# Performance work log

Hardware: AMD Instinct MI355X
Metric: run time of the kernel (lower is better)

## Reference

```python
import jax, jax.numpy as jnp
import numpy as np

N_NODES = 100000
N_EDGES = 1600000
D_IN = 128
D_HID = 128


def setup_inputs() -> dict:
    key = jax.random.key(0)
    ks = jax.random.split(key, 7)
    s_in = 1.0 / np.sqrt(D_IN)
    s_hid = 1.0 / np.sqrt(D_HID)
    return {
        "x": jax.random.normal(ks[0], (N_NODES, D_IN), dtype=jnp.float32),
        "edge_index": jax.random.randint(ks[1], (2, N_EDGES), 0, N_NODES, dtype=jnp.int64),
        "W1_l": jax.random.normal(ks[2], (D_IN, D_HID), dtype=jnp.float32) * s_in,
        "b1": jnp.zeros((D_HID,), dtype=jnp.float32),
        "W1_r": jax.random.normal(ks[3], (D_IN, D_HID), dtype=jnp.float32) * s_in,
        "W2_l": jax.random.normal(ks[4], (D_HID, D_HID), dtype=jnp.float32) * s_hid,
        "b2": jnp.zeros((D_HID,), dtype=jnp.float32),
        "W2_r": jax.random.normal(ks[5], (D_HID, D_HID), dtype=jnp.float32) * s_hid,
    }


def _mean_aggregate(x, src, dst, num_nodes):
    # messages x[src] mean-aggregated at dst (PyG SAGEConv default aggr='mean')
    msg = jnp.take(x, src, axis=0)                       # [E, D] gather
    summed = jax.ops.segment_sum(msg, dst, num_segments=num_nodes)  # [N, D]
    deg = jax.ops.segment_sum(jnp.ones((src.shape[0],), x.dtype), dst,
                              num_segments=num_nodes)
    return summed / jnp.maximum(deg, 1.0)[:, None]


def _sage_conv(x, src, dst, W_l, b, W_r):
    agg = _mean_aggregate(x, src, dst, x.shape[0])
    # out = lin_l(aggregated neighbors) + lin_r(root)
    return agg @ W_l + b + x @ W_r


def reference(x, edge_index, W1_l, b1, W1_r, W2_l, b2, W2_r):
    src, dst = edge_index[0], edge_index[1]
    h = _sage_conv(x, src, dst, W1_l, b1, W1_r)
    h = jax.nn.relu(h)  # dropout inactive in eval mode
    out = _sage_conv(h, src, dst, W2_l, b2, W2_r)
    return out
```

## Files before the change

### kernel.cpp

```cpp
#include <hip/hip_runtime.h>

#define NN 100000
#define NE 1600000
#define DF 128
#define NBUCK 391
#define PA_BLOCKS 196
#define PB_BLOCKS 196
#define CX_BLOCKS 3125
#define CW_BLOCKS 64
#define AGG_GRID 3128

typedef short short8 __attribute__((ext_vector_type(8)));
typedef float floatx4 __attribute__((ext_vector_type(4)));
typedef float floatx2 __attribute__((ext_vector_type(2)));
typedef unsigned int uintx4 __attribute__((ext_vector_type(4)));
typedef unsigned int uintx2 __attribute__((ext_vector_type(2)));
typedef unsigned int uint;
typedef unsigned short ushort;
typedef unsigned char uchar;

static __device__ __forceinline__ ushort f2bf(float f) {
    uint u = __builtin_bit_cast(uint, f);
    return (ushort)((u + 0x7fffu + ((u >> 16) & 1u)) >> 16);
}

__global__ __launch_bounds__(256) void pA_hist(const int* __restrict__ dst,
                                               int* __restrict__ hist,
                                               ushort* __restrict__ rank8) {
    __shared__ int h[NBUCK];
    int tid = threadIdx.x;
    for (int i = tid; i < NBUCK; i += 256) h[i] = 0;
    __syncthreads();
    int eb = blockIdx.x * 8192 + tid;
    #pragma unroll
    for (int k = 0; k < 32; ++k) {
        int e = eb + k * 256;
        if (e < NE) {
            int r = atomicAdd(&h[dst[e] >> 8], 1);
            rank8[e] = (ushort)r;
        }
    }
    __syncthreads();
    int* hrow = hist + blockIdx.x * NBUCK;
    for (int i = tid; i < NBUCK; i += 256) hrow[i] = h[i];
}

__global__ __launch_bounds__(256) void pS2_colscan(int* __restrict__ hist,
                                                   int* __restrict__ gt) {
    __shared__ int ps[256];
    int b = blockIdx.x;
    int tid = threadIdx.x;
    int v = (tid < PA_BLOCKS) ? hist[tid * NBUCK + b] : 0;
    ps[tid] = v;
    __syncthreads();
    for (int st = 1; st < 256; st <<= 1) {
        int t = (tid >= st) ? ps[tid - st] : 0;
        __syncthreads();
        ps[tid] += t;
        __syncthreads();
    }
    if (tid < PA_BLOCKS) hist[tid * NBUCK + b] = ps[tid] - v;
    if (tid == 255) gt[b] = ps[255];
}

__global__ __launch_bounds__(512) void pS_scan(const int* __restrict__ gt,
                                               int* __restrict__ goff) {
    __shared__ int s[512];
    int tid = threadIdx.x;
    int v = (tid < NBUCK) ? gt[tid] : 0;
    s[tid] = v;
    __syncthreads();
    for (int st = 1; st < 512; st <<= 1) {
        int t = (tid >= st) ? s[tid - st] : 0;
        __syncthreads();
        s[tid] += t;
        __syncthreads();
    }
    if (tid < NBUCK) goff[tid] = s[tid] - v;
    if (tid == 0) goff[NBUCK] = NE;
}

__global__ __launch_bounds__(512) void fused_mid(
        const int* __restrict__ src, const int* __restrict__ dst,
        const ushort* __restrict__ rank8, const int* __restrict__ rel,
        const int* __restrict__ goff, uint* __restrict__ pairs,
        const float* __restrict__ x, ushort* __restrict__ xb, uint* __restrict__ xf8,
        const float* __restrict__ W1l, const float* __restrict__ W1r,
        const float* __restrict__ W2l, const float* __restrict__ W2r,
        ushort* __restrict__ WT1, ushort* __restrict__ WT2) {
    __shared__ int lbase[NBUCK];
    int bid = blockIdx.x;
    int tid = threadIdx.x;
    if (bid < PB_BLOCKS) {
        const int* rel_row = rel + bid * NBUCK;
        for (int i = tid; i < NBUCK; i += 512) lbase[i] = goff[i] + rel_row[i];
        __syncthreads();
        int eb = bid * 8192 + tid;
        #pragma unroll
        for (int k = 0; k < 16; ++k) {
            int e = eb + k * 512;
            if (e < NE) {
                int s = src[e];
                int d = dst[e];
                int b = d >> 8;
                int pos = lbase[b] + (int)rank8[e];
                pairs[pos] = ((uint)(d & 255) << 17) | (uint)s;
            }
        }
    } else if (bid < PB_BLOCKS + CX_BLOCKS) {
        int j = (bid - PB_BLOCKS) * 512 + tid;
        const float4* xr = (const float4*)x + (size_t)j * 2;
        float4 v0 = xr[0], v1 = xr[1];
        uintx4 ob;
        ob.x = (uint)f2bf(v0.x) | ((uint)f2bf(v0.y) << 16);
        ob.y = (uint)f2bf(v0.z) | ((uint)f2bf(v0.w) << 16);
        ob.z = (uint)f2bf(v1.x) | ((uint)f2bf(v1.y) << 16);
        ob.w = (uint)f2bf(v1.z) | ((uint)f2bf(v1.w) << 16);
        __builtin_nontemporal_store(ob, (uintx4*)xb + j);
        uint pk0 = (uint)__builtin_amdgcn_cvt_pk_fp8_f32(v0.x, v0.y, 0, false);
        pk0 = (uint)__builtin_amdgcn_cvt_pk_fp8_f32(v0.z, v0.w, (int)pk0, true);
        uint pk1 = (uint)__builtin_amdgcn_cvt_pk_fp8_f32(v1.x, v1.y, 0, false);
        pk1 = (uint)__builtin_amdgcn_cvt_pk_fp8_f32(v1.z, v1.w, (int)pk1, true);
        uintx2 pkv = {pk0, pk1};
        __builtin_nontemporal_store(pkv, (uintx2*)xf8 + j);
    } else {
        int id = (bid - PB_BLOCKS - CX_BLOCKS) * 512 + tid;
        int n = id >> 8, k = id & 255;
        float a = (k < 128) ? W1l[k * 128 + n] : W1r[(k - 128) * 128 + n];
        float b = (k < 128) ? W2l[k * 128 + n] : W2r[(k - 128) * 128 + n];
        WT1[id] = f2bf(a);
        WT2[id] = f2bf(b);
    }
}

__global__ __launch_bounds__(256) void pC_scatter(const uint* __restrict__ pairs,
                                                  const int* __restrict__ goff,
                                                  int* __restrict__ off,
                                                  int* __restrict__ srt) {
    __shared__ int deg[256];
    __shared__ int loc[256];
    int b = blockIdx.x;
    int beg = goff[b], end = goff[b + 1];
    int tid = threadIdx.x;
    deg[tid] = 0;
    __syncthreads();
    for (int i = beg + tid; i < end; i += 256)
        atomicAdd(&deg[pairs[i] >> 17], 1);
    __syncthreads();
    int v = deg[tid];
    loc[tid] = v;
    __syncthreads();
    for (int st = 1; st < 256; st <<= 1) {
        int t = (tid >= st) ? loc[tid - st] : 0;
        __syncthreads();
        loc[tid] += t;
        __syncthreads();
    }
    int excl = loc[tid] - v + beg;
    int n = (b << 8) + tid;
    if (n < NN) off[n] = excl;
    __syncthreads();
    deg[tid] = excl;
    __syncthreads();
    for (int i = beg + tid; i < end; i += 256) {
        uint pr = pairs[i];
        int pos = atomicAdd(&deg[pr >> 17], 1);
        srt[pos] = (int)(pr & 0x1FFFFu);
    }
}

static __device__ __forceinline__ void acc16(floatx2* ac, uint4 v) {
    ac[0] += __builtin_amdgcn_cvt_pk_f32_fp8((int)v.x, false);
    ac[1] += __builtin_amdgcn_cvt_pk_f32_fp8((int)v.x, true);
    ac[2] += __builtin_amdgcn_cvt_pk_f32_fp8((int)v.y, false);
    ac[3] += __builtin_amdgcn_cvt_pk_f32_fp8((int)v.y, true);
    ac[4] += __builtin_amdgcn_cvt_pk_f32_fp8((int)v.z, false);
    ac[5] += __builtin_amdgcn_cvt_pk_f32_fp8((int)v.z, true);
    ac[6] += __builtin_amdgcn_cvt_pk_f32_fp8((int)v.w, false);
    ac[7] += __builtin_amdgcn_cvt_pk_f32_fp8((int)v.w, true);
}

#define AGG_LOOP(IDX)                                            \
    {                                                            \
        int i = lb;                                              \
        for (; i + 8 <= le; i += 8) {                            \
            int idx[8];                                          \
            _Pragma("unroll")                                    \
            for (int k = 0; k < 8; ++k) idx[k] = IDX(i + k);     \
            uint4 v[8];                                          \
            _Pragma("unroll")                                    \
            for (int k = 0; k < 8; ++k) v[k] = f[(size_t)idx[k] * 8]; \
            _Pragma("unroll")                                    \
            for (int k = 0; k < 8; ++k) acc16(ac, v[k]);         \
        }                                                        \
        if (i + 4 <= le) {                                       \
            int idx[4];                                          \
            _Pragma("unroll")                                    \
            for (int k = 0; k < 4; ++k) idx[k] = IDX(i + k);     \
            uint4 v[4];                                          \
            _Pragma("unroll")                                    \
            for (int k = 0; k < 4; ++k) v[k] = f[(size_t)idx[k] * 8]; \
            _Pragma("unroll")                                    \
            for (int k = 0; k < 4; ++k) acc16(ac, v[k]);         \
            i += 4;                                              \
        }                                                        \
        for (; i < le; ++i) {                                    \
            uint4 v = f[(size_t)IDX(i) * 8];                     \
            acc16(ac, v);                                        \
        }                                                        \
    }

__global__ __launch_bounds__(256) void agg_csr(const uint* __restrict__ feat8,
                                               const int* __restrict__ srt,
                                               const int* __restrict__ off,
                                               ushort* __restrict__ aggb) {
    __shared__ int sidx[2048];
    int nb = blockIdx.x * 32;
    if (nb >= NN) return;
    int tid = threadIdx.x;

    int segb = off[nb];
    int nend = nb + 32;
    int sege = (nend < NN) ? off[nend] : NE;
    int stage = min(sege - segb, 2048);
    for (int i = tid; i < stage; i += 256) sidx[i] = srt[segb + i];
    __syncthreads();

    int n = nb + (tid >> 3);
    int l = tid & 7;
    if (n >= NN) return;
    const uint4* f = (const uint4*)feat8 + l;

    int beg = off[n];
    int end = (n < NN - 1) ? off[n + 1] : NE;
    int lb = beg - segb, le = end - segb;

    floatx2 ac[8];
    #pragma unroll
    for (int t = 0; t < 8; ++t) ac[t] = (floatx2){0.f, 0.f};

    if (le <= stage) {
        #define IDX_LDS(ii) sidx[ii]
        AGG_LOOP(IDX_LDS)
        #undef IDX_LDS
    } else {
        #define IDX_GBL(ii) srt[segb + (ii)]
        AGG_LOOP(IDX_GBL)
        #undef IDX_GBL
    }

    float inv = 1.0f / fmaxf((float)(end - beg), 1.0f);
    uintx4 o0, o1;
    o0.x = (uint)f2bf(ac[0].x * inv) | ((uint)f2bf(ac[0].y * inv) << 16);
    o0.y = (uint)f2bf(ac[1].x * inv) | ((uint)f2bf(ac[1].y * inv) << 16);
    o0.z = (uint)f2bf(ac[2].x * inv) | ((uint)f2bf(ac[2].y * inv) << 16);
    o0.w = (uint)f2bf(ac[3].x * inv) | ((uint)f2bf(ac[3].y * inv) << 16);
    o1.x = (uint)f2bf(ac[4].x * inv) | ((uint)f2bf(ac[4].y * inv) << 16);
    o1.y = (uint)f2bf(ac[5].x * inv) | ((uint)f2bf(ac[5].y * inv) << 16);
    o1.z = (uint)f2bf(ac[6].x * inv) | ((uint)f2bf(ac[6].y * inv) << 16);
    o1.w = (uint)f2bf(ac[7].x * inv) | ((uint)f2bf(ac[7].y * inv) << 16);
    uintx4* dp = (uintx4*)(aggb + (size_t)n * 128 + l * 16);
    __builtin_nontemporal_store(o0, dp);
    __builtin_nontemporal_store(o1, dp + 1);
}

template <int RELU, int BF16OUT, int F8OUT>
__global__ __launch_bounds__(512, 4) void gemm_mfma(
        const ushort* __restrict__ aggb, const ushort* __restrict__ selfb,
        const ushort* __restrict__ WT, const float* __restrict__ bias,
        void* __restrict__ outv, uchar* __restrict__ f8out) {
    __shared__ ushort sWT[128 * 256];
    const int tid = threadIdx.x;
    const int blk = blockIdx.x;

    #pragma unroll
    for (int it = 0; it < 8; ++it) {
        int flat = it * 512 + tid;
        int col = flat >> 5;
        int c = flat & 31;
        uint4 v = *(const uint4*)(WT + (size_t)col * 256 + c * 8);
        *(uint4*)&sWT[col * 256 + (c ^ (col & 7)) * 8] = v;
    }

    const int w = tid >> 6;
    const int lane = tid & 63;
    const int m = lane & 15;
    const int q = lane >> 4;

    int node_m = blk * 128 + w * 16 + m;
    int cn = node_m < NN ? node_m : NN - 1;
    const ushort* arow = aggb + (size_t)cn * 128;
    const ushort* xrow = selfb + (size_t)cn * 128;
    short8 a[8];
    #pragma unroll
    for (int kk = 0; kk < 4; ++kk) {
        a[kk]     = *(const short8*)(arow + kk * 32 + q * 8);
        a[4 + kk] = *(const short8*)(xrow + kk * 32 + q * 8);
    }

    __syncthreads();

    floatx4 acc[8];
    #pragma unroll
    for (int t = 0; t < 8; ++t) acc[t] = (floatx4){0.f, 0.f, 0.f, 0.f};

    const int m7 = m & 7;
    #pragma unroll
    for (int kk = 0; kk < 8; ++kk) {
        int cx = (kk * 4 + q) ^ m7;
        #pragma unroll
        for (int t = 0; t < 8; ++t) {
            short8 b = *(const short8*)&sWT[(t * 16 + m) * 256 + cx * 8];
            acc[t] = __builtin_amdgcn_mfma_f32_16x16x32_bf16(a[kk], b, acc[t], 0, 0, 0);
        }
    }

    const int node_base = blk * 128 + w * 16 + q * 4;
    #pragma unroll
    for (int t = 0; t < 8; ++t) {
        int col = t * 16 + m;
        float bj = bias[col];
        #pragma unroll
        for (int r = 0; r < 4; ++r) {
            int node = node_base + r;
            if (node < NN) {
                float v = acc[t][r] + bj;
                if (RELU) v = fmaxf(v, 0.0f);
                if (BF16OUT)
                    ((ushort*)outv)[(size_t)node * 128 + col] = f2bf(v);
                else
                    ((float*)outv)[(size_t)node * 128 + col] = v;
                if (F8OUT) {
                    uint pk = (uint)__builtin_amdgcn_cvt_pk_fp8_f32(v, v, 0, false);
                    f8out[(size_t)node * 128 + col] = (uchar)pk;
                }
            }
        }
    }
}

extern "C" void kernel_launch(void* const* d_in, const int* in_sizes, int n_in,
                              void* d_out, int out_size, void* d_ws, size_t ws_size,
                              hipStream_t stream) {
    const float* x   = (const float*)d_in[0];
    const int*   ei  = (const int*)d_in[1];
    const float* W1l = (const float*)d_in[2];
    const float* b1  = (const float*)d_in[3];
    const float* W1r = (const float*)d_in[4];
    const float* W2l = (const float*)d_in[5];
    const float* b2  = (const float*)d_in[6];
    const float* W2r = (const float*)d_in[7];
    float*       out = (float*)d_out;

    const int* src = ei;
    const int* dst = ei + NE;

    char* ws = (char*)d_ws;
    int*    off  = (int*)(ws);
    int*    srt  = (int*)(ws + 400000);
    ushort* WT1  = (ushort*)(ws + 7200000);
    ushort* WT2  = (ushort*)(ws + 7265536);
    ushort* xb   = (ushort*)(ws + 7331072);
    uint*   xf8  = (uint*)(ws + 32931072);
    ushort* aggb = (ushort*)(ws + 45731072);
    ushort* hb   = (ushort*)(ws + 71331072);
    uchar*  hf8  = (uchar*)xf8;
    uint*   pairs = (uint*)aggb;
    int*    hist  = (int*)((char*)aggb + 6400000);
    ushort* rank8 = (ushort*)((char*)aggb + 6720000);
    int*    gt    = (int*)((char*)aggb + 9920512);
    int*    goff  = (int*)((char*)aggb + 9922304);

    pA_hist<<<PA_BLOCKS, 256, 0, stream>>>(dst, hist, rank8);
    pS2_colscan<<<NBUCK, 256, 0, stream>>>(hist, gt);
    pS_scan<<<1, 512, 0, stream>>>(gt, goff);
    fused_mid<<<PB_BLOCKS + CX_BLOCKS + CW_BLOCKS, 512, 0, stream>>>(
        src, dst, rank8, hist, goff, pairs, x, xb, xf8,
        W1l, W1r, W2l, W2r, WT1, WT2);
    pC_scatter<<<NBUCK, 256, 0, stream>>>(pairs, goff, off, srt);

    const int gemm_grid = (NN + 127) / 128;

    agg_csr<<<AGG_GRID, 256, 0, stream>>>(xf8, srt, off, aggb);
    gemm_mfma<1, 1, 1><<<gemm_grid, 512, 0, stream>>>(aggb, xb, WT1, b1, hb, hf8);

    agg_csr<<<AGG_GRID, 256, 0, stream>>>((const uint*)hf8, srt, off, aggb);
    gemm_mfma<0, 0, 0><<<gemm_grid, 512, 0, stream>>>(aggb, hb, WT2, b2, out, nullptr);
}
```

Before: 181.8 us.

## Stage CSR scatter in LDS, sort neighbor lists, and drop nontemporal stores

The CSR build kernel now scatters each bucket's source indices into shared memory, insertion-sorts each node's neighbor list, and writes the bucket to global memory contiguously. This replaces random global scatter writes with coalesced ones, and sorted neighbor indices should give the gather in aggregation better locality. Separately, the bf16/fp8 conversion stores become regular stores instead of nontemporal ones, so the converted features can stay in cache. The per-thread insertion sort adds serial work proportional to degree squared. The removed early return in agg_csr relies on bounds being safe for the last block, which looks risky since off[n] can be read past NN.

```diff
diff --git a/kernel.cpp b/kernel.cpp
--- a/kernel.cpp
+++ b/kernel.cpp
@@ -9,12 +9,12 @@
 #define CX_BLOCKS 3125
 #define CW_BLOCKS 64
 #define AGG_GRID 3128
+#define PC_LDS 6144
 
 typedef short short8 __attribute__((ext_vector_type(8)));
 typedef float floatx4 __attribute__((ext_vector_type(4)));
 typedef float floatx2 __attribute__((ext_vector_type(2)));
 typedef unsigned int uintx4 __attribute__((ext_vector_type(4)));
-typedef unsigned int uintx2 __attribute__((ext_vector_type(2)));
 typedef unsigned int uint;
 typedef unsigned short ushort;
 typedef unsigned char uchar;
@@ -111,18 +111,17 @@
         int j = (bid - PB_BLOCKS) * 512 + tid;
         const float4* xr = (const float4*)x + (size_t)j * 2;
         float4 v0 = xr[0], v1 = xr[1];
-        uintx4 ob;
+        uint4 ob;
         ob.x = (uint)f2bf(v0.x) | ((uint)f2bf(v0.y) << 16);
         ob.y = (uint)f2bf(v0.z) | ((uint)f2bf(v0.w) << 16);
         ob.z = (uint)f2bf(v1.x) | ((uint)f2bf(v1.y) << 16);
         ob.w = (uint)f2bf(v1.z) | ((uint)f2bf(v1.w) << 16);
-        __builtin_nontemporal_store(ob, (uintx4*)xb + j);
+        ((uint4*)xb)[j] = ob;
         uint pk0 = (uint)__builtin_amdgcn_cvt_pk_fp8_f32(v0.x, v0.y, 0, false);
         pk0 = (uint)__builtin_amdgcn_cvt_pk_fp8_f32(v0.z, v0.w, (int)pk0, true);
         uint pk1 = (uint)__builtin_amdgcn_cvt_pk_fp8_f32(v1.x, v1.y, 0, false);
         pk1 = (uint)__builtin_amdgcn_cvt_pk_fp8_f32(v1.z, v1.w, (int)pk1, true);
-        uintx2 pkv = {pk0, pk1};
-        __builtin_nontemporal_store(pkv, (uintx2*)xf8 + j);
+        ((uint2*)xf8)[j] = make_uint2(pk0, pk1);
     } else {
         int id = (bid - PB_BLOCKS - CX_BLOCKS) * 512 + tid;
         int n = id >> 8, k = id & 255;
@@ -139,8 +138,11 @@
                                                   int* __restrict__ srt) {
     __shared__ int deg[256];
     __shared__ int loc[256];
+    __shared__ int nbase[256];
+    __shared__ int lsrt[PC_LDS];
     int b = blockIdx.x;
     int beg = goff[b], end = goff[b + 1];
+    int seglen = end - beg;
     int tid = threadIdx.x;
     deg[tid] = 0;
     __syncthreads();
@@ -156,16 +158,41 @@
         loc[tid] += t;
         __syncthreads();
     }
-    int excl = loc[tid] - v + beg;
+    int excl = loc[tid] - v;
     int n = (b << 8) + tid;
-    if (n < NN) off[n] = excl;
-    __syncthreads();
-    deg[tid] = excl;
-    __syncthreads();
-    for (int i = beg + tid; i < end; i += 256) {
-        uint pr = pairs[i];
-        int pos = atomicAdd(&deg[pr >> 17], 1);
-        srt[pos] = (int)(pr & 0x1FFFFu);
+    if (n < NN) off[n] = beg + excl;
+    nbase[tid] = excl;
+    __syncthreads();
+    if (seglen <= PC_LDS) {
+        deg[tid] = excl;
+        __syncthreads();
+        for (int i = beg + tid; i < end; i += 256) {
+            uint pr = pairs[i];
+            int pos = atomicAdd(&deg[pr >> 17], 1);
+            lsrt[pos] = (int)(pr & 0x1FFFFu);
+        }
+        __syncthreads();
+        int s0 = nbase[tid], s1 = s0 + v;
+        for (int i = s0 + 1; i < s1; ++i) {
+            int key = lsrt[i];
+            int j = i - 1;
+            while (j >= s0 && lsrt[j] > key) {
+                lsrt[j + 1] = lsrt[j];
+                --j;
+            }
+            lsrt[j + 1] = key;
+        }
+        __syncthreads();
+        for (int i = tid; i < seglen; i += 256)
+            srt[beg + i] = lsrt[i];
+    } else {
+        deg[tid] = beg + excl;
+        __syncthreads();
+        for (int i = beg + tid; i < end; i += 256) {
+            uint pr = pairs[i];
+            int pos = atomicAdd(&deg[pr >> 17], 1);
+            srt[pos] = (int)(pr & 0x1FFFFu);
+        }
     }
 }
 
@@ -228,7 +255,6 @@
 
     int n = nb + (tid >> 3);
     int l = tid & 7;
-    if (n >= NN) return;
     const uint4* f = (const uint4*)feat8 + l;
 
     int beg = off[n];
```

Measured after the change: 216.0 us. 18.8% more time.
